# Kernel tuning notes

Hardware: AMD Instinct MI355X
Metric: run time of the kernel (lower is better)

The kernel has to match this reference:

```python
import jax, jax.numpy as jnp
import numpy as np
from jax import lax
from jax.scipy.special import logsumexp

INSIZE = 256
NBASE = 4
SIZE = 2 * NBASE * (NBASE + 1)  # 40


def setup_inputs() -> dict:
    key = jax.random.key(0)
    kx, kw, kb = jax.random.split(key, 3)
    x = jax.random.normal(kx, (2048, 256, INSIZE), dtype=jnp.float32)
    W = jax.random.normal(kw, (SIZE, INSIZE), dtype=jnp.float32) / np.sqrt(INSIZE)
    b = 0.5 * jax.random.normal(kb, (SIZE,), dtype=jnp.float32)
    return {"x": x, "W": W, "b": b}


def global_norm_flipflop(scores):
    # scores: (T, N, C) with C = 2*nbase*(nbase+1)
    T, N, C = scores.shape
    nbase = int(np.sqrt(C / 2))
    assert 2 * nbase * (nbase + 1) == C

    fwd0 = jnp.zeros((N, 2 * nbase), dtype=scores.dtype)
    logZ0 = logsumexp(fwd0, axis=1, keepdims=True)  # (N, 1) = log(2*nbase)
    fwd0 = fwd0 - logZ0

    def step(carry, sc_t):
        fwd, logZ = carry
        # (N, nbase+1, 2*nbase): transition scores into each destination row
        sc = fwd[:, None, :] + sc_t.reshape(N, nbase + 1, 2 * nbase)
        base1 = logsumexp(sc[:, :nbase], axis=2)  # flip states (N, nbase)
        base2 = jnp.logaddexp(sc[:, nbase, :nbase], sc[:, nbase, nbase:])  # flop (N, nbase)
        new_state = jnp.concatenate([base1, base2], axis=1)  # (N, 2*nbase)
        factors = logsumexp(new_state, axis=1, keepdims=True)
        return (new_state - factors, logZ + factors), None

    (_, logZ), _ = lax.scan(step, (fwd0, logZ0), scores)
    return scores - logZ / T  # broadcast (N,1) over (T,N,C)


def reference(x, W, b):
    y = 5.0 * jnp.tanh(x @ W.T + b)  # (T, N, 40)
    return global_norm_flipflop(y)
```

## Files before the change

### kernel.cpp

```cpp
#include <hip/hip_runtime.h>
#include <hip/hip_bf16.h>

#define T_DIM 2048
#define N_DIM 256
#define K_DIM 256
#define C_DIM 40
#define CHUNK 32
#define NCHUNK 64
#define NSUPER (T_DIM * N_DIM / 64)

#define LOG2E_F 1.44269504088896340736f
#define LN2_F   0.69314718055994530942f
#define NEGBIG  (-1.0e30f)

typedef short bf16x8 __attribute__((ext_vector_type(8)));
typedef float f32x4  __attribute__((ext_vector_type(4)));

__device__ __forceinline__ float fexp2(float x) { return exp2f(x); }
__device__ __forceinline__ float flog2(float x) { return log2f(x); }
__device__ __forceinline__ float frcp(float x) { return __frcp_rn(x); }

__device__ __forceinline__ unsigned int pk2(float a, float b)
{
    __hip_bfloat162 h = __float22bfloat162_rn(make_float2(a, b));
    unsigned int r;
    __builtin_memcpy(&r, &h, sizeof(r));
    return r;
}

__device__ __forceinline__ uint4 pack8u(float4 lo, float4 hi)
{
    uint4 t;
    t.x = pk2(lo.x, lo.y);
    t.y = pk2(lo.z, lo.w);
    t.z = pk2(hi.x, hi.y);
    t.w = pk2(hi.z, hi.w);
    return t;
}

__device__ __forceinline__ bf16x8 as_bf16x8(uint4 u)
{
    bf16x8 r;
    __builtin_memcpy(&r, &u, sizeof(r));
    return r;
}

__device__ __forceinline__ unsigned short bf16r(float v)
{
    return (unsigned short)(pk2(v, 0.0f) & 0xffffu);
}

__device__ __forceinline__ float bl(unsigned int w) { return __uint_as_float(w << 16); }
__device__ __forceinline__ float bh(unsigned int w) { return __uint_as_float(w & 0xffff0000u); }

__device__ __forceinline__ float tanh5(float v)
{
    const float e = fexp2(fabsf(v) * (2.0f * LOG2E_F));
    const float t = 1.0f - 2.0f * frcp(e + 1.0f);
    return 5.0f * copysignf(t, v);
}

__global__ __launch_bounds__(512, 4) void k1_gemm_tanh(
    const float* __restrict__ x, const float* __restrict__ W,
    const float* __restrict__ b, unsigned short* __restrict__ yb)
{
    __shared__ __align__(16) unsigned char xl[64 * 512];
    __shared__ __align__(16) float pl[4 * 12 * 64];

    const int tid  = threadIdx.x;
    const int wave = tid >> 6;
    const int lane = tid & 63;
    const int lr   = lane & 15;
    const int kg   = lane >> 4;
    const int mt   = wave & 3;
    const int kh   = wave >> 2;

    const float bc0 = b[lr];
    const float bc1 = b[16 + lr];
    const float bc2 = (lr < 8) ? b[32 + lr] : 0.0f;

    bf16x8 wf[4][3];
#pragma unroll
    for (int i = 0; i < 4; ++i) {
        const int ks = kh * 4 + i;
#pragma unroll
        for (int nt = 0; nt < 3; ++nt) {
            const int col = nt * 16 + lr;
            float4 lo = make_float4(0, 0, 0, 0), hi = lo;
            if (col < C_DIM) {
                const float* wp = W + (size_t)col * K_DIM + ks * 32 + kg * 8;
                lo = *(const float4*)wp;
                hi = *(const float4*)(wp + 4);
            }
            wf[i][nt] = as_bf16x8(pack8u(lo, hi));
        }
    }

#pragma unroll 1
    for (int st = blockIdx.x; st < NSUPER; st += gridDim.x) {
        const float4* __restrict__ xg4 =
            (const float4*)(x + (size_t)st * 64 * K_DIM);
#pragma unroll
        for (int p = 0; p < 8; ++p) {
            const int f4  = p * 512 + tid;
            const int row = f4 >> 6;
            const int kq  = f4 & 63;
            const float4 v = xg4[f4];
            uint2 w2;
            w2.x = pk2(v.x, v.y);
            w2.y = pk2(v.z, v.w);
            const int off = (row * 512 + kq * 8) ^ ((row & 7) << 4);
            *(uint2*)(xl + off) = w2;
        }
        __syncthreads();

        f32x4 af0, af1, af2;
        if (kh == 0) {
            af0 = (f32x4){bc0, bc0, bc0, bc0};
            af1 = (f32x4){bc1, bc1, bc1, bc1};
            af2 = (f32x4){bc2, bc2, bc2, bc2};
        } else {
            af0 = (f32x4){0.f, 0.f, 0.f, 0.f}; af1 = af0; af2 = af0;
        }
        const int rbase = (mt * 16 + lr) * 512;
        const int swz   = (lr & 7) << 4;
#pragma unroll
        for (int i = 0; i < 4; ++i) {
            const int ks = kh * 4 + i;
            const bf16x8 a =
                *(const bf16x8*)(xl + ((rbase + ks * 64 + kg * 16) ^ swz));
            af0 = __builtin_amdgcn_mfma_f32_16x16x32_bf16(a, wf[i][0], af0, 0, 0, 0);
            af1 = __builtin_amdgcn_mfma_f32_16x16x32_bf16(a, wf[i][1], af1, 0, 0, 0);
            af2 = __builtin_amdgcn_mfma_f32_16x16x32_bf16(a, wf[i][2], af2, 0, 0, 0);
        }

        if (kh == 1) {
            float* p = pl + (mt * 12) * 64 + lane;
#pragma unroll
            for (int j = 0; j < 4; ++j) p[j * 64]       = af0[j];
#pragma unroll
            for (int j = 0; j < 4; ++j) p[(4 + j) * 64] = af1[j];
#pragma unroll
            for (int j = 0; j < 4; ++j) p[(8 + j) * 64] = af2[j];
        }
        __syncthreads();

        if (kh == 0) {
            const float* p = pl + (mt * 12) * 64 + lane;
            unsigned short* yr =
                yb + ((size_t)st * 64 + mt * 16 + kg * 4) * C_DIM;
#pragma unroll
            for (int r = 0; r < 4; ++r) {
                yr[r * C_DIM + lr]      = bf16r(tanh5(af0[r] + p[r * 64]));
                yr[r * C_DIM + 16 + lr] = bf16r(tanh5(af1[r] + p[(4 + r) * 64]));
                if (lr < 8)
                    yr[r * C_DIM + 32 + lr] = bf16r(tanh5(af2[r] + p[(8 + r) * 64]));
            }
        }
    }
}

__global__ __launch_bounds__(256) void k2_chunks(
    const unsigned short* __restrict__ yb, float* __restrict__ cmat)
{
    const int tid  = threadIdx.x;
    const int wave = tid >> 6;
    const int lane = tid & 63;
    const int task = lane >> 3;
    const int c    = lane & 7;
    const int g    = blockIdx.x & (NCHUNK - 1);
    const int n    = ((blockIdx.x >> 6) << 5) + (wave << 3) + task;

    float col[8];
#pragma unroll
    for (int j = 0; j < 8; ++j) col[j] = (j == c) ? 0.0f : NEGBIG;

    const unsigned short* __restrict__ yp =
        yb + ((size_t)(g * CHUNK) * N_DIM + (size_t)n) * C_DIM;

#pragma unroll 1
    for (int s = 0; s < CHUNK; ++s) {
        float sc[C_DIM];
        const uint4* p4 = (const uint4*)yp;
#pragma unroll
        for (int q = 0; q < 5; ++q) {
            const uint4 u = p4[q];
            sc[8 * q + 0] = bl(u.x) * LOG2E_F;
            sc[8 * q + 1] = bh(u.x) * LOG2E_F;
            sc[8 * q + 2] = bl(u.y) * LOG2E_F;
            sc[8 * q + 3] = bh(u.y) * LOG2E_F;
            sc[8 * q + 4] = bl(u.z) * LOG2E_F;
            sc[8 * q + 5] = bh(u.z) * LOG2E_F;
            sc[8 * q + 6] = bl(u.w) * LOG2E_F;
            sc[8 * q + 7] = bh(u.w) * LOG2E_F;
        }
        float nc[8];
#pragma unroll
        for (int d = 0; d < 4; ++d) {
            float tv[8];
#pragma unroll
            for (int j = 0; j < 8; ++j) tv[j] = sc[d * 8 + j] + col[j];
            float m = tv[0];
#pragma unroll
            for (int j = 1; j < 8; ++j) m = fmaxf(m, tv[j]);
            float ss = 0.0f;
#pragma unroll
            for (int j = 0; j < 8; ++j) ss += fexp2(tv[j] - m);
            nc[d] = m + flog2(ss);
        }
#pragma unroll
        for (int i = 0; i < 4; ++i) {
            const float a  = sc[32 + i] + col[i];
            const float bb = sc[36 + i] + col[i + 4];
            const float m  = fmaxf(a, bb);
            const float ss = fexp2(a - m) + fexp2(bb - m);
            nc[4 + i] = m + flog2(ss);
        }
#pragma unroll
        for (int j = 0; j < 8; ++j) col[j] = nc[j];
        yp += (size_t)N_DIM * C_DIM;
    }
    float* __restrict__ op = cmat + (((size_t)g * 8 + c) * N_DIM + n) * 8;
#pragma unroll
    for (int j = 0; j < 8; ++j) op[j] = col[j];
}

__global__ __launch_bounds__(256) void k3_combine(
    const float* __restrict__ cmat, float* __restrict__ corr)
{
    const int tid = threadIdx.x;
    const int d   = tid & 7;
    const int n   = blockIdx.x * 32 + (tid >> 3);

    float v[8];
#pragma unroll
    for (int j = 0; j < 8; ++j) v[j] = 0.0f;

#pragma unroll 1
    for (int g = 0; g < NCHUNK; ++g) {
        const float* mg = cmat + ((size_t)g * 8 * N_DIM + n) * 8 + d;
        float mm[8];
#pragma unroll
        for (int j = 0; j < 8; ++j) mm[j] = mg[(size_t)j * N_DIM * 8];
        float tv[8];
#pragma unroll
        for (int j = 0; j < 8; ++j) tv[j] = mm[j] + v[j];
        float m = tv[0];
#pragma unroll
        for (int j = 1; j < 8; ++j) m = fmaxf(m, tv[j]);
        float ss = 0.0f;
#pragma unroll
        for (int j = 0; j < 8; ++j) ss += fexp2(tv[j] - m);
        const float nv = m + flog2(ss);
#pragma unroll
        for (int j = 0; j < 8; ++j) v[j] = __shfl(nv, j, 8);
    }
    float m = v[0];
#pragma unroll
    for (int j = 1; j < 8; ++j) m = fmaxf(m, v[j]);
    float ss = 0.0f;
#pragma unroll
    for (int j = 0; j < 8; ++j) ss += fexp2(v[j] - m);
    const float lz2 = m + flog2(ss);
    if (d == 0) corr[n] = lz2 * LN2_F / (float)T_DIM;
}

__global__ __launch_bounds__(256) void k4_final(
    const unsigned short* __restrict__ yb, const float* __restrict__ corr,
    float* __restrict__ out)
{
    const int i = blockIdx.x * 256 + threadIdx.x;
    const uint4 u = ((const uint4*)yb)[i];
    const float cr = corr[(i / 5) & (N_DIM - 1)];
    float4 o0, o1;
    o0.x = bl(u.x) - cr; o0.y = bh(u.x) - cr;
    o0.z = bl(u.y) - cr; o0.w = bh(u.y) - cr;
    o1.x = bl(u.z) - cr; o1.y = bh(u.z) - cr;
    o1.z = bl(u.w) - cr; o1.w = bh(u.w) - cr;
    float4* o4 = (float4*)out;
    o4[i * 2]     = o0;
    o4[i * 2 + 1] = o1;
}

extern "C" void kernel_launch(void* const* d_in, const int* in_sizes, int n_in,
                              void* d_out, int out_size, void* d_ws, size_t ws_size,
                              hipStream_t stream)
{
    const float* x = (const float*)d_in[0];
    const float* W = (const float*)d_in[1];
    const float* b = (const float*)d_in[2];
    float* out = (float*)d_out;

    unsigned short* ybf = (unsigned short*)d_ws;
    float* cmat = (float*)((char*)d_ws + (48u << 20));
    float* corr = cmat + (size_t)NCHUNK * 8 * N_DIM * 8;

    hipLaunchKernelGGL(k1_gemm_tanh, dim3(1024), dim3(512), 0, stream, x, W, b, ybf);
    hipLaunchKernelGGL(k2_chunks,    dim3(512),  dim3(256), 0, stream, ybf, cmat);
    hipLaunchKernelGGL(k3_combine,   dim3(8),    dim3(256), 0, stream, cmat, corr);
    hipLaunchKernelGGL(k4_final,     dim3(T_DIM * N_DIM * C_DIM / 8 / 256),
                       dim3(256), 0, stream, ybf, corr, out);
}
```

Before: 253.2 us.

## Prepack W fragments and drop split-K waves in GEMM-tanh kernel

Adds a tiny pre-kernel that converts W to bf16 MFMA fragment layout in workspace, and restructures the GEMM kernel to 256 threads where each wave does the full K=256 reduction instead of splitting K across two wave halves. This removes the LDS partial-sum exchange, one barrier and the idle half of waves during tanh/store, at the cost of reloading W fragments from global/L2 inside the loop and having fewer threads per block to stage the x tile. The per-kernel W conversion also moves out of every block's prologue.

```diff
diff --git a/kernel.cpp b/kernel.cpp
--- a/kernel.cpp
+++ b/kernel.cpp
@@ -60,49 +60,52 @@
     return 5.0f * copysignf(t, v);
 }
 
-__global__ __launch_bounds__(512, 4) void k1_gemm_tanh(
-    const float* __restrict__ x, const float* __restrict__ W,
+__global__ __launch_bounds__(256) void k0_pack(
+    const float* __restrict__ W, uint4* __restrict__ wfrag)
+{
+    const int f    = blockIdx.x * 256 + threadIdx.x;
+    const int l    = f & 63;
+    const int frag = f >> 6;
+    const int nt   = frag % 3;
+    const int ks   = frag / 3;
+    const int col  = nt * 16 + (l & 15);
+    const int kg   = l >> 4;
+    float4 lo = make_float4(0, 0, 0, 0), hi = lo;
+    if (col < C_DIM) {
+        const float* wp = W + (size_t)col * K_DIM + ks * 32 + kg * 8;
+        lo = *(const float4*)wp;
+        hi = *(const float4*)(wp + 4);
+    }
+    wfrag[frag * 64 + l] = pack8u(lo, hi);
+}
+
+__global__ __launch_bounds__(256, 4) void k1_gemm_tanh(
+    const float* __restrict__ x, const uint4* __restrict__ wfrag,
     const float* __restrict__ b, unsigned short* __restrict__ yb)
 {
     __shared__ __align__(16) unsigned char xl[64 * 512];
-    __shared__ __align__(16) float pl[4 * 12 * 64];
 
     const int tid  = threadIdx.x;
     const int wave = tid >> 6;
     const int lane = tid & 63;
     const int lr   = lane & 15;
     const int kg   = lane >> 4;
-    const int mt   = wave & 3;
-    const int kh   = wave >> 2;
+    const int mt   = wave;
 
     const float bc0 = b[lr];
     const float bc1 = b[16 + lr];
     const float bc2 = (lr < 8) ? b[32 + lr] : 0.0f;
 
-    bf16x8 wf[4][3];
-#pragma unroll
-    for (int i = 0; i < 4; ++i) {
-        const int ks = kh * 4 + i;
-#pragma unroll
-        for (int nt = 0; nt < 3; ++nt) {
-            const int col = nt * 16 + lr;
-            float4 lo = make_float4(0, 0, 0, 0), hi = lo;
-            if (col < C_DIM) {
-                const float* wp = W + (size_t)col * K_DIM + ks * 32 + kg * 8;
-                lo = *(const float4*)wp;
-                hi = *(const float4*)(wp + 4);
-            }
-            wf[i][nt] = as_bf16x8(pack8u(lo, hi));
-        }
-    }
+    const int rbase = (mt * 16 + lr) * 512;
+    const int swz   = (lr & 7) << 4;
 
 #pragma unroll 1
-    for (int st = blockIdx.x; st < NSUPER; st += gridDim.x) {
+    for (int st = blockIdx.x; st < NSUPER; st += 1024) {
         const float4* __restrict__ xg4 =
             (const float4*)(x + (size_t)st * 64 * K_DIM);
 #pragma unroll
-        for (int p = 0; p < 8; ++p) {
-            const int f4  = p * 512 + tid;
+        for (int p = 0; p < 16; ++p) {
+            const int f4  = p * 256 + tid;
             const int row = f4 >> 6;
             const int kq  = f4 & 63;
             const float4 v = xg4[f4];
@@ -114,49 +117,33 @@
         }
         __syncthreads();
 
-        f32x4 af0, af1, af2;
-        if (kh == 0) {
-            af0 = (f32x4){bc0, bc0, bc0, bc0};
-            af1 = (f32x4){bc1, bc1, bc1, bc1};
-            af2 = (f32x4){bc2, bc2, bc2, bc2};
-        } else {
-            af0 = (f32x4){0.f, 0.f, 0.f, 0.f}; af1 = af0; af2 = af0;
-        }
-        const int rbase = (mt * 16 + lr) * 512;
-        const int swz   = (lr & 7) << 4;
-#pragma unroll
-        for (int i = 0; i < 4; ++i) {
-            const int ks = kh * 4 + i;
+        f32x4 af0 = {bc0, bc0, bc0, bc0};
+        f32x4 af1 = {bc1, bc1, bc1, bc1};
+        f32x4 af2 = {bc2, bc2, bc2, bc2};
+
+#pragma unroll
+        for (int ks = 0; ks < 8; ++ks) {
             const bf16x8 a =
                 *(const bf16x8*)(xl + ((rbase + ks * 64 + kg * 16) ^ swz));
-            af0 = __builtin_amdgcn_mfma_f32_16x16x32_bf16(a, wf[i][0], af0, 0, 0, 0);
-            af1 = __builtin_amdgcn_mfma_f32_16x16x32_bf16(a, wf[i][1], af1, 0, 0, 0);
-            af2 = __builtin_amdgcn_mfma_f32_16x16x32_bf16(a, wf[i][2], af2, 0, 0, 0);
-        }
-
-        if (kh == 1) {
-            float* p = pl + (mt * 12) * 64 + lane;
-#pragma unroll
-            for (int j = 0; j < 4; ++j) p[j * 64]       = af0[j];
-#pragma unroll
-            for (int j = 0; j < 4; ++j) p[(4 + j) * 64] = af1[j];
-#pragma unroll
-            for (int j = 0; j < 4; ++j) p[(8 + j) * 64] = af2[j];
+            const uint4* wp = wfrag + (ks * 3) * 64 + lane;
+            const bf16x8 w0 = as_bf16x8(wp[0]);
+            const bf16x8 w1 = as_bf16x8(wp[64]);
+            const bf16x8 w2 = as_bf16x8(wp[128]);
+            af0 = __builtin_amdgcn_mfma_f32_16x16x32_bf16(a, w0, af0, 0, 0, 0);
+            af1 = __builtin_amdgcn_mfma_f32_16x16x32_bf16(a, w1, af1, 0, 0, 0);
+            af2 = __builtin_amdgcn_mfma_f32_16x16x32_bf16(a, w2, af2, 0, 0, 0);
+        }
+
+        unsigned short* yr =
+            yb + ((size_t)st * 64 + mt * 16 + kg * 4) * C_DIM;
+#pragma unroll
+        for (int r = 0; r < 4; ++r) {
+            yr[r * C_DIM + lr]      = bf16r(tanh5(af0[r]));
+            yr[r * C_DIM + 16 + lr] = bf16r(tanh5(af1[r]));
+            if (lr < 8)
+                yr[r * C_DIM + 32 + lr] = bf16r(tanh5(af2[r]));
         }
         __syncthreads();
-
-        if (kh == 0) {
-            const float* p = pl + (mt * 12) * 64 + lane;
-            unsigned short* yr =
-                yb + ((size_t)st * 64 + mt * 16 + kg * 4) * C_DIM;
-#pragma unroll
-            for (int r = 0; r < 4; ++r) {
-                yr[r * C_DIM + lr]      = bf16r(tanh5(af0[r] + p[r * 64]));
-                yr[r * C_DIM + 16 + lr] = bf16r(tanh5(af1[r] + p[(4 + r) * 64]));
-                if (lr < 8)
-                    yr[r * C_DIM + 32 + lr] = bf16r(tanh5(af2[r] + p[(8 + r) * 64]));
-            }
-        }
     }
 }
 
@@ -294,8 +281,10 @@
     unsigned short* ybf = (unsigned short*)d_ws;
     float* cmat = (float*)((char*)d_ws + (48u << 20));
     float* corr = cmat + (size_t)NCHUNK * 8 * N_DIM * 8;
-
-    hipLaunchKernelGGL(k1_gemm_tanh, dim3(1024), dim3(512), 0, stream, x, W, b, ybf);
+    uint4* wfrag = (uint4*)((char*)d_ws + (56u << 20));
+
+    hipLaunchKernelGGL(k0_pack,      dim3(6),    dim3(256), 0, stream, W, wfrag);
+    hipLaunchKernelGGL(k1_gemm_tanh, dim3(1024), dim3(256), 0, stream, x, wfrag, b, ybf);
     hipLaunchKernelGGL(k2_chunks,    dim3(512),  dim3(256), 0, stream, ybf, cmat);
     hipLaunchKernelGGL(k3_combine,   dim3(8),    dim3(256), 0, stream, cmat, corr);
     hipLaunchKernelGGL(k4_final,     dim3(T_DIM * N_DIM * C_DIM / 8 / 256),
```

Result: slower. 302.6 us (+19.5%).

## Double-buffer x tiles in GEMM-tanh kernel with register prefetch of next tile

Applied to the files above, without the earlier changes.

Converts the persistent GEMM loop to a software pipeline: the next 64-row x tile is loaded into registers before the MFMA and tanh work on the current tile, then packed into a second LDS buffer afterwards. This hides global load latency behind compute. In exchange it uses more registers and doubles the x LDS footprint, which may lower occupancy, and it hardcodes a grid stride of 1024 and 8 iterations per block.

```diff
diff --git a/kernel.cpp b/kernel.cpp
--- a/kernel.cpp
+++ b/kernel.cpp
@@ -64,7 +64,7 @@
     const float* __restrict__ x, const float* __restrict__ W,
     const float* __restrict__ b, unsigned short* __restrict__ yb)
 {
-    __shared__ __align__(16) unsigned char xl[64 * 512];
+    __shared__ __align__(16) unsigned char xl[2][64 * 512];
     __shared__ __align__(16) float pl[4 * 12 * 64];
 
     const int tid  = threadIdx.x;
@@ -96,23 +96,45 @@
         }
     }
 
-#pragma unroll 1
-    for (int st = blockIdx.x; st < NSUPER; st += gridDim.x) {
+    int soff[8];
+#pragma unroll
+    for (int p = 0; p < 8; ++p) {
+        const int f4  = p * 512 + tid;
+        const int row = f4 >> 6;
+        const int kq  = f4 & 63;
+        soff[p] = (row * 512 + kq * 8) ^ ((row & 7) << 4);
+    }
+
+    const int rbase = (mt * 16 + lr) * 512;
+    const int swz   = (lr & 7) << 4;
+
+    int st = blockIdx.x;
+    float4 v[8];
+    {
         const float4* __restrict__ xg4 =
             (const float4*)(x + (size_t)st * 64 * K_DIM);
 #pragma unroll
+        for (int p = 0; p < 8; ++p) v[p] = xg4[p * 512 + tid];
+#pragma unroll
         for (int p = 0; p < 8; ++p) {
-            const int f4  = p * 512 + tid;
-            const int row = f4 >> 6;
-            const int kq  = f4 & 63;
-            const float4 v = xg4[f4];
             uint2 w2;
-            w2.x = pk2(v.x, v.y);
-            w2.y = pk2(v.z, v.w);
-            const int off = (row * 512 + kq * 8) ^ ((row & 7) << 4);
-            *(uint2*)(xl + off) = w2;
-        }
-        __syncthreads();
+            w2.x = pk2(v[p].x, v[p].y);
+            w2.y = pk2(v[p].z, v[p].w);
+            *(uint2*)(xl[0] + soff[p]) = w2;
+        }
+    }
+    __syncthreads();
+
+    int cur = 0;
+#pragma unroll 1
+    for (int t = 0; t < 8; ++t, st += 1024) {
+        const bool have_next = (t + 1 < 8);
+        if (have_next) {
+            const float4* __restrict__ xg4 =
+                (const float4*)(x + (size_t)(st + 1024) * 64 * K_DIM);
+#pragma unroll
+            for (int p = 0; p < 8; ++p) v[p] = xg4[p * 512 + tid];
+        }
 
         f32x4 af0, af1, af2;
         if (kh == 0) {
@@ -122,13 +144,12 @@
         } else {
             af0 = (f32x4){0.f, 0.f, 0.f, 0.f}; af1 = af0; af2 = af0;
         }
-        const int rbase = (mt * 16 + lr) * 512;
-        const int swz   = (lr & 7) << 4;
+        const unsigned char* xb = xl[cur];
 #pragma unroll
         for (int i = 0; i < 4; ++i) {
             const int ks = kh * 4 + i;
             const bf16x8 a =
-                *(const bf16x8*)(xl + ((rbase + ks * 64 + kg * 16) ^ swz));
+                *(const bf16x8*)(xb + ((rbase + ks * 64 + kg * 16) ^ swz));
             af0 = __builtin_amdgcn_mfma_f32_16x16x32_bf16(a, wf[i][0], af0, 0, 0, 0);
             af1 = __builtin_amdgcn_mfma_f32_16x16x32_bf16(a, wf[i][1], af1, 0, 0, 0);
             af2 = __builtin_amdgcn_mfma_f32_16x16x32_bf16(a, wf[i][2], af2, 0, 0, 0);
@@ -157,6 +178,19 @@
                     yr[r * C_DIM + 32 + lr] = bf16r(tanh5(af2[r] + p[(8 + r) * 64]));
             }
         }
+
+        if (have_next) {
+            unsigned char* xn = xl[cur ^ 1];
+#pragma unroll
+            for (int p = 0; p < 8; ++p) {
+                uint2 w2;
+                w2.x = pk2(v[p].x, v[p].y);
+                w2.y = pk2(v[p].z, v[p].w);
+                *(uint2*)(xn + soff[p]) = w2;
+            }
+        }
+        __syncthreads();
+        cur ^= 1;
     }
 }
 
```

Measured after the change: 354.0 us. 1.4x slower.

## Double-buffer x tiles via async global_load_lds in GEMM-tanh kernel

Applied to the files above, without the earlier changes.

Rewrites the first kernel to stream 32-row tiles of x straight into LDS as fp32 with global_load_lds, using two buffers so the next tile's load overlaps the MFMA and tanh work on the current one. The bf16 conversion now happens at fragment read time instead of at store time. Blocks shrink to 256 threads with a fixed grid of 512 looping 32 times. This targets exposed global-load latency in a bandwidth-bound GEMM, at the cost of twice the LDS footprint per row, manual waitcnt/barrier handling that could race if the counts are wrong, and lower occupancy.

```diff
diff --git a/kernel.cpp b/kernel.cpp
--- a/kernel.cpp
+++ b/kernel.cpp
@@ -7,7 +7,7 @@
 #define C_DIM 40
 #define CHUNK 32
 #define NCHUNK 64
-#define NSUPER (T_DIM * N_DIM / 64)
+#define NT32 (T_DIM * N_DIM / 32)
 
 #define LOG2E_F 1.44269504088896340736f
 #define LN2_F   0.69314718055994530942f
@@ -60,20 +60,20 @@
     return 5.0f * copysignf(t, v);
 }
 
-__global__ __launch_bounds__(512, 4) void k1_gemm_tanh(
+__global__ __launch_bounds__(256, 2) void k1_gemm_tanh(
     const float* __restrict__ x, const float* __restrict__ W,
     const float* __restrict__ b, unsigned short* __restrict__ yb)
 {
-    __shared__ __align__(16) unsigned char xl[64 * 512];
-    __shared__ __align__(16) float pl[4 * 12 * 64];
+    __shared__ __align__(16) float xl[2][32 * 256];
+    __shared__ __align__(16) float pl[2][12 * 64];
 
     const int tid  = threadIdx.x;
     const int wave = tid >> 6;
     const int lane = tid & 63;
     const int lr   = lane & 15;
     const int kg   = lane >> 4;
-    const int mt   = wave & 3;
-    const int kh   = wave >> 2;
+    const int mt   = wave & 1;
+    const int kh   = wave >> 1;
 
     const float bc0 = b[lr];
     const float bc1 = b[16 + lr];
@@ -96,23 +96,32 @@
         }
     }
 
+#define STAGE(buf, st_)                                                        \
+    {                                                                          \
+        _Pragma("unroll")                                                      \
+        for (int p = 0; p < 8; ++p) {                                          \
+            const int r = wave * 8 + p;                                        \
+            const float* gp = x + ((size_t)(st_) * 32 + r) * 256               \
+                                + ((lane ^ (r & 7)) << 2);                     \
+            __builtin_amdgcn_global_load_lds(                                  \
+                (const __attribute__((address_space(1))) unsigned int*)gp,     \
+                (__attribute__((address_space(3))) unsigned int*)&xl[buf][r * 256], \
+                16, 0, 0);                                                     \
+        }                                                                      \
+    }
+
+    const int rr = mt * 16 + lr;
+    const int sw = lr & 7;
+
+    int st = blockIdx.x;
+    STAGE(0, st)
+    asm volatile("s_waitcnt vmcnt(0)" ::: "memory");
+    __builtin_amdgcn_s_barrier();
+
+    int cur = 0;
 #pragma unroll 1
-    for (int st = blockIdx.x; st < NSUPER; st += gridDim.x) {
-        const float4* __restrict__ xg4 =
-            (const float4*)(x + (size_t)st * 64 * K_DIM);
-#pragma unroll
-        for (int p = 0; p < 8; ++p) {
-            const int f4  = p * 512 + tid;
-            const int row = f4 >> 6;
-            const int kq  = f4 & 63;
-            const float4 v = xg4[f4];
-            uint2 w2;
-            w2.x = pk2(v.x, v.y);
-            w2.y = pk2(v.z, v.w);
-            const int off = (row * 512 + kq * 8) ^ ((row & 7) << 4);
-            *(uint2*)(xl + off) = w2;
-        }
-        __syncthreads();
+    for (int t = 0; t < 32; ++t, st += 512) {
+        if (t + 1 < 32) STAGE(cur ^ 1, st + 512)
 
         f32x4 af0, af1, af2;
         if (kh == 0) {
@@ -122,20 +131,20 @@
         } else {
             af0 = (f32x4){0.f, 0.f, 0.f, 0.f}; af1 = af0; af2 = af0;
         }
-        const int rbase = (mt * 16 + lr) * 512;
-        const int swz   = (lr & 7) << 4;
+        const float* rowp = &xl[cur][rr * 256];
 #pragma unroll
         for (int i = 0; i < 4; ++i) {
-            const int ks = kh * 4 + i;
-            const bf16x8 a =
-                *(const bf16x8*)(xl + ((rbase + ks * 64 + kg * 16) ^ swz));
+            const int u0 = (kh * 4 + i) * 8 + kg * 2;
+            const float4 lo = *(const float4*)(rowp + ((u0 ^ sw) << 2));
+            const float4 hi = *(const float4*)(rowp + (((u0 + 1) ^ sw) << 2));
+            const bf16x8 a = as_bf16x8(pack8u(lo, hi));
             af0 = __builtin_amdgcn_mfma_f32_16x16x32_bf16(a, wf[i][0], af0, 0, 0, 0);
             af1 = __builtin_amdgcn_mfma_f32_16x16x32_bf16(a, wf[i][1], af1, 0, 0, 0);
             af2 = __builtin_amdgcn_mfma_f32_16x16x32_bf16(a, wf[i][2], af2, 0, 0, 0);
         }
 
         if (kh == 1) {
-            float* p = pl + (mt * 12) * 64 + lane;
+            float* p = &pl[mt][lane];
 #pragma unroll
             for (int j = 0; j < 4; ++j) p[j * 64]       = af0[j];
 #pragma unroll
@@ -143,12 +152,13 @@
 #pragma unroll
             for (int j = 0; j < 4; ++j) p[(8 + j) * 64] = af2[j];
         }
-        __syncthreads();
+        asm volatile("s_waitcnt lgkmcnt(0)" ::: "memory");
+        __builtin_amdgcn_s_barrier();
 
         if (kh == 0) {
-            const float* p = pl + (mt * 12) * 64 + lane;
+            const float* p = &pl[mt][lane];
             unsigned short* yr =
-                yb + ((size_t)st * 64 + mt * 16 + kg * 4) * C_DIM;
+                yb + ((size_t)st * 32 + mt * 16 + kg * 4) * C_DIM;
 #pragma unroll
             for (int r = 0; r < 4; ++r) {
                 yr[r * C_DIM + lr]      = bf16r(tanh5(af0[r] + p[r * 64]));
@@ -156,8 +166,14 @@
                 if (lr < 8)
                     yr[r * C_DIM + 32 + lr] = bf16r(tanh5(af2[r] + p[(8 + r) * 64]));
             }
-        }
-    }
+            asm volatile("s_waitcnt vmcnt(12)" ::: "memory");
+        } else {
+            asm volatile("s_waitcnt vmcnt(0)" ::: "memory");
+        }
+        __builtin_amdgcn_s_barrier();
+        cur ^= 1;
+    }
+#undef STAGE
 }
 
 __global__ __launch_bounds__(256) void k2_chunks(
@@ -295,7 +311,7 @@
     float* cmat = (float*)((char*)d_ws + (48u << 20));
     float* corr = cmat + (size_t)NCHUNK * 8 * N_DIM * 8;
 
-    hipLaunchKernelGGL(k1_gemm_tanh, dim3(1024), dim3(512), 0, stream, x, W, b, ybf);
+    hipLaunchKernelGGL(k1_gemm_tanh, dim3(512),  dim3(256), 0, stream, x, W, b, ybf);
     hipLaunchKernelGGL(k2_chunks,    dim3(512),  dim3(256), 0, stream, ybf, cmat);
     hipLaunchKernelGGL(k3_combine,   dim3(8),    dim3(256), 0, stream, cmat, corr);
     hipLaunchKernelGGL(k4_final,     dim3(T_DIM * N_DIM * C_DIM / 8 / 256),
```

After: 246.6 us. -2.6%, faster.
